# Performance work log

Measured on AMD Instinct MI355X. Metric: run time of the kernel, lower is better.

The kernel has to match this reference:

```python
import jax, jax.numpy as jnp
import numpy as np

NUM_BLOCKS = 2
NUM_LAYERS = 10
L = NUM_BLOCKS * NUM_LAYERS  # 20 wave layers
C_IN, C_RES, C_SKIP = 8, 64, 256
B, T = 32, 4096


def causal_conv1d(x, w, b, dilation=1):
    # x: [B, C_in, T], w: [C_out, C_in, K], left-pad so output is causal and length-preserving
    k = w.shape[2]
    out = jax.lax.conv_general_dilated(
        x, w, window_strides=(1,), padding=[(dilation * (k - 1), 0)],
        rhs_dilation=(dilation,), dimension_numbers=("NCH", "OIH", "NCH"))
    return out + b[None, :, None]


def setup_inputs() -> dict:
    key = jax.random.key(0)
    ks = jax.random.split(key, 12)
    s1 = 1.0 / np.sqrt(C_IN)
    s2 = 1.0 / np.sqrt(2 * C_RES)
    s3 = 1.0 / np.sqrt(C_RES)
    return {
        "x":    jax.random.normal(ks[0], (B, C_IN, T), jnp.float32),
        "w_in": jax.random.normal(ks[1], (C_RES, C_IN, 1), jnp.float32) * s1,
        "b_in": jax.random.normal(ks[2], (C_RES,), jnp.float32) * s1,
        "w_f":  jax.random.normal(ks[3], (L, C_RES, C_RES, 2), jnp.float32) * s2,
        "b_f":  jax.random.normal(ks[4], (L, C_RES), jnp.float32) * s2,
        "w_g":  jax.random.normal(ks[5], (L, C_RES, C_RES, 2), jnp.float32) * s2,
        "b_g":  jax.random.normal(ks[6], (L, C_RES), jnp.float32) * s2,
        "w_s":  jax.random.normal(ks[7], (L, C_SKIP, C_RES, 1), jnp.float32) * s3,
        "b_s":  jax.random.normal(ks[8], (L, C_SKIP), jnp.float32) * s3,
        "w_r":  jax.random.normal(ks[9], (L, C_RES, C_RES, 1), jnp.float32) * s3,
        "b_r":  jax.random.normal(ks[10], (L, C_RES), jnp.float32) * s3,
    }


def reference(x, w_in, b_in, w_f, b_f, w_g, b_g, w_s, b_s, w_r, b_r):
    # WaveNet.encode: 1x1 input conv, then num_blocks*num_layers gated dilated causal layers
    h = causal_conv1d(x, w_in, b_in)            # [B, C_RES, T]
    skips = jnp.zeros((x.shape[0], w_s.shape[1], x.shape[2]), x.dtype)
    for i in range(L):
        d = 2 ** (i % NUM_LAYERS)
        f = jnp.tanh(causal_conv1d(h, w_f[i], b_f[i], d))
        g = jax.nn.sigmoid(causal_conv1d(h, w_g[i], b_g[i], d))
        z = f * g                                # gated activation
        skips = skips + causal_conv1d(z, w_s[i], b_s[i])
        h = h + causal_conv1d(z, w_r[i], b_r[i])  # residual connection
    return skips
```

## Files before the change

### kernel.cpp

```cpp
#include <hip/hip_runtime.h>

#define B_ 32
#define T_ 4096
#define CR 64
#define CS 256
#define NL 20

typedef __bf16 bf16x8 __attribute__((ext_vector_type(8)));
typedef __bf16 bf16x4v __attribute__((ext_vector_type(4)));
typedef float f32x4 __attribute__((ext_vector_type(4)));

__device__ __forceinline__ f32x4 mfma16(bf16x8 a, bf16x8 b, f32x4 c) {
  return __builtin_amdgcn_mfma_f32_16x16x32_bf16(a, b, c, 0, 0, 0);
}

__global__ void pack_kernel(const float* __restrict__ wf, const float* __restrict__ wg,
                            const float* __restrict__ wsn, const float* __restrict__ wr,
                            const float* __restrict__ bs,
                            __bf16* __restrict__ Wfg2, __bf16* __restrict__ Wr2,
                            __bf16* __restrict__ Ws2, float* __restrict__ bsS) {
  int n = blockIdx.x * 256 + threadIdx.x;
  if (n < 327680) {
    int j = n & 7, lane = (n >> 3) & 63, fr = (n >> 9) & 7, mt = (n >> 12) & 3, i = n >> 14;
    int cs = mt * 16 + (lane & 15);
    int k = (fr & 3) * 32 + (lane >> 4) * 8 + j;
    int ci = k & 63, tap = k >> 6;
    const float* src = (fr < 4) ? wf : wg;
    Wfg2[n] = (__bf16)src[((i * 64 + cs) * 64 + ci) * 2 + tap];
  } else if (n < 409600) {
    int m = n - 327680;
    int j = m & 7, lane = (m >> 3) & 63, kc = (m >> 9) & 1, mt = (m >> 10) & 3, i = m >> 12;
    int cs = mt * 16 + (lane & 15);
    int ci = kc * 32 + (lane >> 4) * 8 + j;
    Wr2[m] = (__bf16)wr[(i * 64 + cs) * 64 + ci];
  } else if (n < 737280) {
    int m = n - 409600;
    int j = m & 7, lane = (m >> 3) & 63, kc = (m >> 9) & 1, tile = (m >> 10) & 15, i = m >> 14;
    int cs = tile * 16 + (lane & 15);
    int ci = kc * 32 + (lane >> 4) * 8 + j;
    Ws2[m] = (__bf16)wsn[i * 16384 + cs * 64 + ci];
  } else if (n < 737536) {
    int cs = n - 737280;
    float s = 0.f;
    for (int i = 0; i < NL; ++i) s += bs[i * 256 + cs];
    bsS[cs] = s;
  }
}

__global__ void inconv_kernel(const float* __restrict__ x, const float* __restrict__ w_in,
                              const float* __restrict__ b_in, float* __restrict__ h0) {
  __shared__ float w[64][8];
  __shared__ float bi[64];
  int tid = threadIdx.x;
  for (int k = tid; k < 512; k += 256) w[k >> 3][k & 7] = w_in[k];
  if (tid < 64) bi[tid] = b_in[tid];
  __syncthreads();
  int b = blockIdx.x >> 4;
  int t = ((blockIdx.x & 15) << 8) + tid;
  float xv[8];
#pragma unroll
  for (int ci = 0; ci < 8; ++ci) xv[ci] = x[((size_t)b * 8 + ci) * T_ + t];
  float* orow = h0 + ((size_t)b * T_ + t) * 64;
#pragma unroll
  for (int c0 = 0; c0 < 64; c0 += 4) {
    float s0 = bi[c0], s1 = bi[c0 + 1], s2 = bi[c0 + 2], s3 = bi[c0 + 3];
#pragma unroll
    for (int ci = 0; ci < 8; ++ci) {
      s0 += w[c0][ci] * xv[ci];
      s1 += w[c0 + 1][ci] * xv[ci];
      s2 += w[c0 + 2][ci] * xv[ci];
      s3 += w[c0 + 3][ci] * xv[ci];
    }
    float4 o = make_float4(s0, s1, s2, s3);
    *(float4*)(orow + c0) = o;
  }
}

__global__ __launch_bounds__(256) void layer_kernel(
    const float* __restrict__ h_in, float* __restrict__ h_out,
    const __bf16* __restrict__ Wfg, const __bf16* __restrict__ Wr,
    const float* __restrict__ bF, const float* __restrict__ bG,
    const float* __restrict__ bR,
    __bf16* __restrict__ Zg, int d, int il, int Gs) {
  __shared__ __bf16 sB[2][64][72];

  const int tid = threadIdx.x;
  const int b = blockIdx.x >> 6;
  const int t0 = (blockIdx.x & 63) << 6;
  const float* hbase = h_in + ((size_t)b * T_ + t0) * 64;

#pragma unroll
  for (int it = 0; it < 4; ++it) {
    int f = (it * 256 + tid) * 4;
    int tr = f >> 6, c = f & 63;
    float4 v = *(const float4*)(hbase + tr * 64 + c);
    bf16x4v pc = {(__bf16)v.x, (__bf16)v.y, (__bf16)v.z, (__bf16)v.w};
    *(bf16x4v*)&sB[1][tr][c] = pc;
    int td = t0 + tr - d;
    float4 u = make_float4(0.f, 0.f, 0.f, 0.f);
    if (td >= 0) u = *(const float4*)(h_in + ((size_t)b * T_ + td) * 64 + c);
    bf16x4v pd = {(__bf16)u.x, (__bf16)u.y, (__bf16)u.z, (__bf16)u.w};
    *(bf16x4v*)&sB[0][tr][c] = pd;
  }
  __syncthreads();

  const int lane = tid & 63, wid = tid >> 6;
  const int tl = (wid << 4) | (lane & 15);
  const int kq = lane >> 4;

  bf16x8 bh[4];
  bh[0] = *(const bf16x8*)&sB[0][tl][kq * 8];
  bh[1] = *(const bf16x8*)&sB[0][tl][32 + kq * 8];
  bh[2] = *(const bf16x8*)&sB[1][tl][kq * 8];
  bh[3] = *(const bf16x8*)&sB[1][tl][32 + kq * 8];

  __bf16 (*sZ)[72] = sB[0];

#pragma unroll
  for (int mt = 0; mt < 4; ++mt) {
    const __bf16* wb = Wfg + (mt * 8) * 512 + lane * 8;
    f32x4 aF = {0.f, 0.f, 0.f, 0.f}, aG = {0.f, 0.f, 0.f, 0.f};
#pragma unroll
    for (int kc = 0; kc < 4; ++kc) {
      aF = mfma16(*(const bf16x8*)(wb + kc * 512), bh[kc], aF);
      aG = mfma16(*(const bf16x8*)(wb + (4 + kc) * 512), bh[kc], aG);
    }
    const int c0 = (mt << 4) + (kq << 2);
    float4 bfv = *(const float4*)(bF + c0);
    float4 bgv = *(const float4*)(bG + c0);
    float fb[4] = {bfv.x, bfv.y, bfv.z, bfv.w};
    float gb[4] = {bgv.x, bgv.y, bgv.z, bgv.w};
    bf16x4v zv;
#pragma unroll
    for (int r = 0; r < 4; ++r) {
      float fp = aF[r] + fb[r];
      float gp = aG[r] + gb[r];
      float e = __expf(2.f * fp);
      float th = 1.f - 2.f / (e + 1.f);
      float sg = 1.f / (1.f + __expf(-gp));
      zv[r] = (__bf16)(th * sg);
    }
    *(bf16x4v*)&sZ[tl][c0] = zv;
  }

  bf16x8 bz0 = *(const bf16x8*)&sZ[tl][kq * 8];
  bf16x8 bz1 = *(const bf16x8*)&sZ[tl][32 + kq * 8];
#pragma unroll
  for (int mt = 0; mt < 4; ++mt) {
    const __bf16* wrb = Wr + (mt * 2) * 512 + lane * 8;
    f32x4 aR = {0.f, 0.f, 0.f, 0.f};
    aR = mfma16(*(const bf16x8*)(wrb), bz0, aR);
    aR = mfma16(*(const bf16x8*)(wrb + 512), bz1, aR);
    const int c0 = (mt << 4) + (kq << 2);
    float4 hv = *(const float4*)(h_in + ((size_t)b * T_ + t0 + tl) * 64 + c0);
    float4 brv = *(const float4*)(bR + c0);
    float4 o;
    o.x = hv.x + aR[0] + brv.x;
    o.y = hv.y + aR[1] + brv.y;
    o.z = hv.z + aR[2] + brv.z;
    o.w = hv.w + aR[3] + brv.w;
    *(float4*)(h_out + ((size_t)b * T_ + t0 + tl) * 64 + c0) = o;
  }

  __syncthreads();
  {
    int tr = tid >> 2, ch = (tid & 3) << 4;
    const uint4 v0 = *(const uint4*)&sZ[tr][ch];
    const uint4 v1 = *(const uint4*)&sZ[tr][ch + 8];
    __bf16* dst = Zg + (((size_t)b * T_ + t0 + tr) * Gs + il) * 64 + ch;
    *(uint4*)dst = v0;
    *(uint4*)(dst + 8) = v1;
  }
}

__global__ __launch_bounds__(256) void skip_kernel(
    const __bf16* __restrict__ Zg, const __bf16* __restrict__ Ws2,
    const float* __restrict__ bsS, float* __restrict__ out,
    int i0, int cnt, int Gs, int first) {
  __shared__ __bf16 sZ[2][64][72];

  const int tid = threadIdx.x;
  const int b = blockIdx.x >> 6;
  const int t0 = (blockIdx.x & 63) << 6;
  const int lane = tid & 63, wid = tid >> 6;
  const int kq = lane >> 4;
  const int tr = tid >> 2, coff = (tid & 3) << 4;

  const __bf16* zbase = Zg + (((size_t)b * T_ + t0 + tr) * Gs) * 64 + coff;
  const __bf16* wbase = Ws2 + (size_t)i0 * 16384 + (size_t)(wid * 8) * 512 + lane * 8;

  {
    uint4 z0 = *(const uint4*)zbase;
    uint4 z1 = *(const uint4*)(zbase + 8);
    *(uint4*)&sZ[0][tr][coff] = z0;
    *(uint4*)&sZ[0][tr][coff + 8] = z1;
  }
  bf16x8 aw[8];
#pragma unroll
  for (int f = 0; f < 8; ++f) aw[f] = *(const bf16x8*)(wbase + f * 512);

  f32x4 acc[16];
#pragma unroll
  for (int q = 0; q < 16; ++q) acc[q] = (f32x4){0.f, 0.f, 0.f, 0.f};

  __syncthreads();

  const char* zrow0 = (const char*)&sZ[0][0][0] + (lane & 15) * 144 + kq * 16;

  for (int il = 0; il < cnt; ++il) {
    const int cur = il & 1;
    bf16x8 bz[8];
#pragma unroll
    for (int nt = 0; nt < 4; ++nt) {
      bz[nt * 2]     = *(const bf16x8*)(zrow0 + cur * 9216 + nt * 2304);
      bz[nt * 2 + 1] = *(const bf16x8*)(zrow0 + cur * 9216 + nt * 2304 + 64);
    }
    uint4 p0, p1;
    bf16x8 awn[8];
    const bool more = (il + 1) < cnt;
    if (more) {
      p0 = *(const uint4*)(zbase + (il + 1) * 64);
      p1 = *(const uint4*)(zbase + (il + 1) * 64 + 8);
#pragma unroll
      for (int f = 0; f < 8; ++f)
        awn[f] = *(const bf16x8*)(wbase + (size_t)(il + 1) * 16384 + f * 512);
    }
#pragma unroll
    for (int mt = 0; mt < 4; ++mt) {
#pragma unroll
      for (int nt = 0; nt < 4; ++nt) {
        acc[mt * 4 + nt] = mfma16(aw[mt * 2], bz[nt * 2], acc[mt * 4 + nt]);
        acc[mt * 4 + nt] = mfma16(aw[mt * 2 + 1], bz[nt * 2 + 1], acc[mt * 4 + nt]);
      }
    }
    if (more) {
      *(uint4*)&sZ[cur ^ 1][tr][coff] = p0;
      *(uint4*)&sZ[cur ^ 1][tr][coff + 8] = p1;
#pragma unroll
      for (int f = 0; f < 8; ++f) aw[f] = awn[f];
      __syncthreads();
    }
  }

  const int csb = wid * 64 + (kq << 2);
  const int tcol = t0 + (lane & 15);
#pragma unroll
  for (int mt = 0; mt < 4; ++mt) {
#pragma unroll
    for (int nt = 0; nt < 4; ++nt) {
#pragma unroll
      for (int r = 0; r < 4; ++r) {
        int cs = csb + mt * 16 + r;
        size_t idx = ((size_t)b * CS + cs) * T_ + tcol + nt * 16;
        float v = acc[mt * 4 + nt][r];
        if (first) out[idx] = v + bsS[cs];
        else out[idx] += v;
      }
    }
  }
}

extern "C" void kernel_launch(void* const* d_in, const int* in_sizes, int n_in,
                              void* d_out, int out_size, void* d_ws, size_t ws_size,
                              hipStream_t stream) {
  (void)in_sizes; (void)n_in; (void)out_size;
  const float* x    = (const float*)d_in[0];
  const float* w_in = (const float*)d_in[1];
  const float* b_in = (const float*)d_in[2];
  const float* w_f  = (const float*)d_in[3];
  const float* b_f  = (const float*)d_in[4];
  const float* w_g  = (const float*)d_in[5];
  const float* b_g  = (const float*)d_in[6];
  const float* w_s  = (const float*)d_in[7];
  const float* b_s  = (const float*)d_in[8];
  const float* w_r  = (const float*)d_in[9];
  const float* b_r  = (const float*)d_in[10];
  float* out = (float*)d_out;

  char* ws = (char*)d_ws;
  size_t off = 0;
  auto alloc = [&](size_t bytes) -> char* {
    char* p = ws + off;
    off = (off + bytes + 255) & ~(size_t)255;
    return p;
  };
  float* hA = (float*)alloc((size_t)B_ * T_ * 64 * 4);
  float* hB = (float*)alloc((size_t)B_ * T_ * 64 * 4);
  __bf16* Wfg2 = (__bf16*)alloc((size_t)NL * 16384 * 2);
  __bf16* Wr2  = (__bf16*)alloc((size_t)NL * 4096 * 2);
  __bf16* Ws2  = (__bf16*)alloc((size_t)NL * 16384 * 2);
  float* bsS = (float*)alloc(CS * 4);

  size_t zslot = (size_t)B_ * T_ * 64 * 2;
  size_t rem = (ws_size > off) ? (ws_size - off) : 0;
  int G = (int)(rem / zslot);
  if (G > NL) G = NL;
  if (G < 1) G = 1;
  __bf16* Zg = (__bf16*)(ws + off);

  hipLaunchKernelGGL(pack_kernel, dim3(2881), dim3(256), 0, stream,
                     w_f, w_g, w_s, w_r, b_s, Wfg2, Wr2, Ws2, bsS);
  hipLaunchKernelGGL(inconv_kernel, dim3(512), dim3(256), 0, stream, x, w_in, b_in, hA);

  float* hc = hA;
  float* hn = hB;
  int i0 = 0;
  for (int i = 0; i < NL; ++i) {
    int il = i - i0;
    hipLaunchKernelGGL(layer_kernel, dim3(B_ * 64), dim3(256), 0, stream,
                       hc, hn, Wfg2 + (size_t)i * 16384, Wr2 + (size_t)i * 4096,
                       b_f + i * 64, b_g + i * 64, b_r + i * 64,
                       Zg, 1 << (i % 10), il, G);
    { float* tmp = hc; hc = hn; hn = tmp; }
    if (il + 1 == G || i == NL - 1) {
      int cnt = il + 1;
      hipLaunchKernelGGL(skip_kernel, dim3(B_ * 64), dim3(256), 0, stream,
                         Zg, Ws2, bsS, out, i0, cnt, G, (i0 == 0) ? 1 : 0);
      i0 = i + 1;
    }
  }
}
```

Measured before the change: 1.005 ms.

## Swizzle layer block order, write Z directly, deepen skip-kernel prefetch pipeline

The layer kernel now remaps block indices so consecutive blocks spread across batches. It issues all h loads before converting them into shared memory, and writes the gated Z values straight to global from registers, which drops the trailing barrier and the shared-memory copy-out. The skip kernel prefetches Z two steps ahead and weights one step ahead. It replaces __syncthreads with a bare LDS-wait plus s_barrier under sched_barrier fences, to overlap global latency with MFMA work. The gains come with more register pressure, and the direct Z stores are narrower (8-byte) per thread.

```diff
diff --git a/kernel.cpp b/kernel.cpp
--- a/kernel.cpp
+++ b/kernel.cpp
@@ -85,22 +85,29 @@
   __shared__ __bf16 sB[2][64][72];
 
   const int tid = threadIdx.x;
-  const int b = blockIdx.x >> 6;
-  const int t0 = (blockIdx.x & 63) << 6;
+  const int bid = ((blockIdx.x & 7) << 8) | (blockIdx.x >> 3);
+  const int b = bid >> 6;
+  const int t0 = (bid & 63) << 6;
   const float* hbase = h_in + ((size_t)b * T_ + t0) * 64;
 
+  float4 vc[4], vd[4];
 #pragma unroll
   for (int it = 0; it < 4; ++it) {
     int f = (it * 256 + tid) * 4;
-    int tr = f >> 6, c = f & 63;
-    float4 v = *(const float4*)(hbase + tr * 64 + c);
-    bf16x4v pc = {(__bf16)v.x, (__bf16)v.y, (__bf16)v.z, (__bf16)v.w};
-    *(bf16x4v*)&sB[1][tr][c] = pc;
-    int td = t0 + tr - d;
-    float4 u = make_float4(0.f, 0.f, 0.f, 0.f);
-    if (td >= 0) u = *(const float4*)(h_in + ((size_t)b * T_ + td) * 64 + c);
-    bf16x4v pd = {(__bf16)u.x, (__bf16)u.y, (__bf16)u.z, (__bf16)u.w};
-    *(bf16x4v*)&sB[0][tr][c] = pd;
+    int trr = f >> 6, c = f & 63;
+    vc[it] = *(const float4*)(hbase + trr * 64 + c);
+    int td = t0 + trr - d;
+    vd[it] = make_float4(0.f, 0.f, 0.f, 0.f);
+    if (td >= 0) vd[it] = *(const float4*)(h_in + ((size_t)b * T_ + td) * 64 + c);
+  }
+#pragma unroll
+  for (int it = 0; it < 4; ++it) {
+    int f = (it * 256 + tid) * 4;
+    int trr = f >> 6, c = f & 63;
+    bf16x4v pc = {(__bf16)vc[it].x, (__bf16)vc[it].y, (__bf16)vc[it].z, (__bf16)vc[it].w};
+    *(bf16x4v*)&sB[1][trr][c] = pc;
+    bf16x4v pd = {(__bf16)vd[it].x, (__bf16)vd[it].y, (__bf16)vd[it].z, (__bf16)vd[it].w};
+    *(bf16x4v*)&sB[0][trr][c] = pd;
   }
   __syncthreads();
 
@@ -115,6 +122,7 @@
   bh[3] = *(const bf16x8*)&sB[1][tl][32 + kq * 8];
 
   __bf16 (*sZ)[72] = sB[0];
+  __bf16* zrow = Zg + (((size_t)b * T_ + t0 + tl) * Gs + il) * 64;
 
 #pragma unroll
   for (int mt = 0; mt < 4; ++mt) {
@@ -141,6 +149,7 @@
       zv[r] = (__bf16)(th * sg);
     }
     *(bf16x4v*)&sZ[tl][c0] = zv;
+    *(bf16x4v*)(zrow + c0) = zv;
   }
 
   bf16x8 bz0 = *(const bf16x8*)&sZ[tl][kq * 8];
@@ -161,16 +170,6 @@
     o.w = hv.w + aR[3] + brv.w;
     *(float4*)(h_out + ((size_t)b * T_ + t0 + tl) * 64 + c0) = o;
   }
-
-  __syncthreads();
-  {
-    int tr = tid >> 2, ch = (tid & 3) << 4;
-    const uint4 v0 = *(const uint4*)&sZ[tr][ch];
-    const uint4 v1 = *(const uint4*)&sZ[tr][ch + 8];
-    __bf16* dst = Zg + (((size_t)b * T_ + t0 + tr) * Gs + il) * 64 + ch;
-    *(uint4*)dst = v0;
-    *(uint4*)(dst + 8) = v1;
-  }
 }
 
 __global__ __launch_bounds__(256) void skip_kernel(
@@ -189,41 +188,52 @@
   const __bf16* zbase = Zg + (((size_t)b * T_ + t0 + tr) * Gs) * 64 + coff;
   const __bf16* wbase = Ws2 + (size_t)i0 * 16384 + (size_t)(wid * 8) * 512 + lane * 8;
 
-  {
-    uint4 z0 = *(const uint4*)zbase;
-    uint4 z1 = *(const uint4*)(zbase + 8);
-    *(uint4*)&sZ[0][tr][coff] = z0;
-    *(uint4*)&sZ[0][tr][coff + 8] = z1;
-  }
+  uint4 a0 = *(const uint4*)zbase;
+  uint4 a1 = *(const uint4*)(zbase + 8);
   bf16x8 aw[8];
 #pragma unroll
   for (int f = 0; f < 8; ++f) aw[f] = *(const bf16x8*)(wbase + f * 512);
+  uint4 p0 = {0, 0, 0, 0}, p1 = {0, 0, 0, 0};
+  if (cnt > 1) {
+    p0 = *(const uint4*)(zbase + 64);
+    p1 = *(const uint4*)(zbase + 72);
+  }
+  *(uint4*)&sZ[0][tr][coff] = a0;
+  *(uint4*)&sZ[0][tr][coff + 8] = a1;
 
   f32x4 acc[16];
 #pragma unroll
   for (int q = 0; q < 16; ++q) acc[q] = (f32x4){0.f, 0.f, 0.f, 0.f};
 
-  __syncthreads();
+  asm volatile("s_waitcnt lgkmcnt(0)" ::: "memory");
+  __builtin_amdgcn_sched_barrier(0);
+  __builtin_amdgcn_s_barrier();
+  __builtin_amdgcn_sched_barrier(0);
 
   const char* zrow0 = (const char*)&sZ[0][0][0] + (lane & 15) * 144 + kq * 16;
 
   for (int il = 0; il < cnt; ++il) {
     const int cur = il & 1;
+    const bool have1 = (il + 1) < cnt;
+    const bool have2 = (il + 2) < cnt;
+
+    bf16x8 awn[8];
+    if (have1) {
+#pragma unroll
+      for (int f = 0; f < 8; ++f)
+        awn[f] = *(const bf16x8*)(wbase + (size_t)(il + 1) * 16384 + f * 512);
+    }
+    uint4 q0, q1;
+    if (have2) {
+      q0 = *(const uint4*)(zbase + (size_t)(il + 2) * 64);
+      q1 = *(const uint4*)(zbase + (size_t)(il + 2) * 64 + 8);
+    }
+
     bf16x8 bz[8];
 #pragma unroll
     for (int nt = 0; nt < 4; ++nt) {
       bz[nt * 2]     = *(const bf16x8*)(zrow0 + cur * 9216 + nt * 2304);
       bz[nt * 2 + 1] = *(const bf16x8*)(zrow0 + cur * 9216 + nt * 2304 + 64);
-    }
-    uint4 p0, p1;
-    bf16x8 awn[8];
-    const bool more = (il + 1) < cnt;
-    if (more) {
-      p0 = *(const uint4*)(zbase + (il + 1) * 64);
-      p1 = *(const uint4*)(zbase + (il + 1) * 64 + 8);
-#pragma unroll
-      for (int f = 0; f < 8; ++f)
-        awn[f] = *(const bf16x8*)(wbase + (size_t)(il + 1) * 16384 + f * 512);
     }
 #pragma unroll
     for (int mt = 0; mt < 4; ++mt) {
@@ -233,12 +243,17 @@
         acc[mt * 4 + nt] = mfma16(aw[mt * 2 + 1], bz[nt * 2 + 1], acc[mt * 4 + nt]);
       }
     }
-    if (more) {
+
+    if (have1) {
       *(uint4*)&sZ[cur ^ 1][tr][coff] = p0;
       *(uint4*)&sZ[cur ^ 1][tr][coff + 8] = p1;
+      if (have2) { p0 = q0; p1 = q1; }
 #pragma unroll
       for (int f = 0; f < 8; ++f) aw[f] = awn[f];
-      __syncthreads();
+      asm volatile("s_waitcnt lgkmcnt(0)" ::: "memory");
+      __builtin_amdgcn_sched_barrier(0);
+      __builtin_amdgcn_s_barrier();
+      __builtin_amdgcn_sched_barrier(0);
     }
   }
 
```

New measurement: 1.011 ms. No clear change (+0.6%).
